# Optimization experiments

Measured on AMD Instinct MI355X. Metric: run time of the kernel, lower is better.

The kernel has to match this reference:

```python
import jax, jax.numpy as jnp
import numpy as np

NUM_QUERIES = 150
NEG = 1e9


def setup_inputs() -> dict:
    key = jax.random.key(0)
    ks = jax.random.split(key, 5)
    B, C, H, W = 4, 256, 64, 64
    img_feat = jax.random.normal(ks[0], (B, C, H, W), dtype=jnp.float32)
    exe_feat = jax.random.normal(ks[1], (B, C), dtype=jnp.float32)
    mask = jax.random.bernoulli(ks[2], 0.9, (B, H, W)).astype(jnp.float32)
    # similarity initialized as identity (plus tiny noise so it's non-degenerate)
    similarity = jnp.eye(C, dtype=jnp.float32) + 0.01 * jax.random.normal(ks[3], (C, C), dtype=jnp.float32)
    # nn.Linear weight, shape (out, in)
    v_w = jax.random.normal(ks[4], (C, C), dtype=jnp.float32) / np.sqrt(C)
    return {"img_feat": img_feat, "exe_feat": exe_feat, "mask": mask,
            "similarity": similarity, "v_w": v_w}


def _get_queries(attn, B, H, W):
    # peak detection on similarity-to-exemplar channel (last column), no grad
    simil = jax.lax.stop_gradient(attn[:, :, -1]).reshape(B, H, W)
    c = simil[:, 1:-1, 1:-1]
    is_max = ((c > simil[:, :-2, 1:-1]) &   # strictly greater than above
              (c >= simil[:, 2:, 1:-1]) &   # >= below
              (c > simil[:, 1:-1, :-2]) &   # strictly greater than left
              (c >= simil[:, 1:-1, 2:]))    # >= right
    pen = jnp.zeros_like(simil).at[:, 1:-1, 1:-1].set(
        jnp.where(is_max, 0.0, NEG))
    scores = (simil - pen).reshape(B, H * W)
    _, q_ids = jax.lax.top_k(scores, NUM_QUERIES)  # [B, Q]
    return q_ids


def reference(img_feat, exe_feat, mask, similarity, v_w):
    B, C, H, W = img_feat.shape
    HW = H * W
    unrolled = img_feat.reshape(B, C, HW)                      # [B,C,HW]
    exe = (exe_feat * 1.2)[:, :, None]                         # [B,C,1]
    concat = jnp.concatenate([unrolled, exe], axis=2)          # [B,C,HW+1]
    # values = Linear(concat^T): x @ W^T
    values = jnp.einsum('bcn,dc->bnd', concat, v_w)            # [B,HW+1,C]
    # attn = unrolled^T @ similarity @ concat
    attn = jnp.einsum('bcn,cd,bdm->bnm', unrolled, similarity, concat)  # [B,HW,HW+1]

    q_ids = _get_queries(attn, B, H, W)                        # [B,Q] int
    queries = jnp.take_along_axis(values[:, :-1], q_ids[:, :, None], axis=1)  # [B,Q,C]

    # masked softmax: outer product of pixel mask, exemplar column always kept
    m = jax.lax.stop_gradient(mask).reshape(B, HW)
    mm = m[:, :, None] * m[:, None, :]                         # [B,HW,HW]
    mm = jnp.concatenate([mm, jnp.ones((B, HW, 1), mm.dtype)], axis=2)
    attn = attn - (mm != 1).astype(attn.dtype) * NEG
    attn = jax.nn.softmax(attn, axis=2)

    new_img = jnp.einsum('bnm,bmd->bnd', attn, values)         # [B,HW,C]
    new_img = new_img.transpose(0, 2, 1).reshape(B, C, H, W)
    return new_img + img_feat, queries
```

## Files before the change

### kernel.cpp

```cpp
#include <hip/hip_runtime.h>

#define CC   256
#define HWS  4096
#define MPAD 4160
#define NB   4
#define NTIL 65

typedef __attribute__((ext_vector_type(8))) short   short8;
typedef __attribute__((ext_vector_type(4))) float   floatx4;

static __device__ __forceinline__ short8 ld8(const unsigned short* p) {
  return *(const short8*)p;
}
static __device__ __forceinline__ void st8(unsigned short* p, short8 v) {
  *(short8*)p = v;
}
static __device__ __forceinline__ unsigned short f2b(float x) {
  union { float f; unsigned u; } v; v.f = x;
  unsigned r = v.u + 0x7FFFu + ((v.u >> 16) & 1u);
  return (unsigned short)(r >> 16);
}
static __device__ __forceinline__ float b2f(unsigned short x) {
  union { unsigned u; float f; } v; v.u = ((unsigned)x) << 16;
  return v.f;
}

__global__ void prep_colb(const float* __restrict__ sim, const float* __restrict__ vw,
                          const float* __restrict__ mask,
                          unsigned short* __restrict__ St, unsigned short* __restrict__ Vw,
                          float* __restrict__ colb) {
  int blk = blockIdx.x, tid = threadIdx.x;
  if (blk < CC) {
    int dd = blk, c = tid;
    St[dd*CC + c] = f2b(sim[c*CC + dd]);
    Vw[dd*CC + c] = f2b(vw[dd*CC + c]);
    return;
  }
  int b = blk - CC;
  for (int m = tid; m < MPAD; m += 256) {
    float v;
    if (m < HWS)      v = (mask[b*HWS + m] - 1.0f) * 1e9f;
    else if (m == HWS) v = 0.0f;
    else               v = -3.0e38f;
    colb[b*MPAD + m] = v;
  }
}

__global__ void build_kt(const float* __restrict__ img, const float* __restrict__ exe,
                         unsigned short* __restrict__ Kt, unsigned short* __restrict__ Kf) {
  int b = blockIdx.x, mt = blockIdx.y, dt = blockIdx.z;
  int tid = threadIdx.x;
  int m0 = mt*64, d0 = dt*64;
  int w = tid >> 6, lane = tid & 63, lo = lane & 15, hi = lane >> 4;
  unsigned short* kft = Kf + (size_t)(b*NTIL + mt)*16384;
  if (mt == 64) {
    for (int i = 0; i < 16; ++i) {
      int m = m0 + (tid>>6) + i*4;
      int d = d0 + (tid&63);
      unsigned short v = 0;
      if (m == 4096) v = f2b(1.2f * exe[b*CC + d]);
      Kt[((size_t)b*MPAD + m)*CC + d] = v;
    }
#pragma unroll
    for (int ss = 0; ss < 2; ++ss) {
      int s = dt*8 + w*2 + ss;
      int k = s >> 2, t = s & 3;
      unsigned short tmp[8] = {0,0,0,0,0,0,0,0};
      if (t == 0 && lo == 0) {
#pragma unroll
        for (int j = 0; j < 8; ++j)
          tmp[j] = f2b(1.2f * exe[b*CC + k*32 + hi*8 + j]);
      }
      st8(kft + s*512 + lane*8, *(short8*)tmp);
    }
    return;
  }
  __shared__ float tile[64][65];
  for (int i = 0; i < 16; ++i) {
    int dl = (tid>>6) + i*4, ml = tid&63;
    tile[dl][ml] = img[((size_t)b*CC + d0+dl)*HWS + m0+ml];
  }
  __syncthreads();
  for (int i = 0; i < 16; ++i) {
    int ml = (tid>>6) + i*4, dl = tid&63;
    Kt[((size_t)b*MPAD + m0+ml)*CC + d0+dl] = f2b(tile[dl][ml]);
  }
#pragma unroll
  for (int ss = 0; ss < 2; ++ss) {
    int s = dt*8 + w*2 + ss;
    int k = s >> 2, t = s & 3;
    int ml = t*16 + lo;
    int dlb = (k - dt*2)*32 + hi*8;
    unsigned short tmp[8];
#pragma unroll
    for (int j = 0; j < 8; ++j) tmp[j] = f2b(tile[dlb + j][ml]);
    st8(kft + s*512 + lane*8, *(short8*)tmp);
  }
}

__global__ __launch_bounds__(256) void gemm_small(const unsigned short* __restrict__ Kt,
    const unsigned short* __restrict__ Bm, unsigned short* __restrict__ Tout,
    unsigned short* __restrict__ Vf, int mode) {
  int b  = blockIdx.x;
  int r0 = blockIdx.y*64 + (threadIdx.x>>6)*16;
  int c0 = blockIdx.z*64;
  int lane = threadIdx.x & 63;
  int lo = lane & 15, hi = lane >> 4;
  floatx4 acc[4] = {};
  const unsigned short* arow = Kt + ((size_t)b*MPAD + r0 + lo)*CC + hi*8;
#pragma unroll
  for (int k = 0; k < 8; ++k) {
    short8 af = ld8(arow + k*32);
#pragma unroll
    for (int t = 0; t < 4; ++t) {
      short8 bf = ld8(Bm + (size_t)(c0 + t*16 + lo)*CC + k*32 + hi*8);
      acc[t] = __builtin_amdgcn_mfma_f32_16x16x32_bf16(af, bf, acc[t], 0, 0, 0);
    }
  }
  if (mode == 0) {
#pragma unroll
    for (int t = 0; t < 4; ++t)
#pragma unroll
      for (int r = 0; r < 4; ++r) {
        int n = r0 + hi*4 + r, dd = c0 + t*16 + lo;
        Tout[((size_t)b*HWS + n)*CC + dd] = f2b(acc[t][r]);
      }
  } else {
    unsigned short* vfb = Vf + (size_t)b*NTIL*16384;
#pragma unroll
    for (int t = 0; t < 4; ++t)
#pragma unroll
      for (int r = 0; r < 4; ++r) {
        int m = r0 + hi*4 + r, dd = c0 + t*16 + lo;
        int mt = m >> 6, ml = m & 63;
        int h = ml >> 5, im = ml & 31;
        int s = h*16 + (dd >> 4);
        int lane2 = (im >> 3)*16 + lo;
        int j = im & 7;
        vfb[(size_t)mt*16384 + s*512 + lane2*8 + j] = f2b(acc[t][r]);
      }
  }
}

__global__ __launch_bounds__(256) void scores_kernel(const float* __restrict__ img,
    const float* __restrict__ sim, const float* __restrict__ exe,
    float* __restrict__ score32) {
  int b = blockIdx.x, n0 = blockIdx.y*32;
  int d = threadIdx.x;
  __shared__ float U[32][257];
  __shared__ float R[32][257];
  __shared__ float E[256];
  for (int idx = threadIdx.x; idx < 32*256; idx += 256) {
    int nl = idx & 31, c = idx >> 5;
    U[nl][c] = img[((size_t)b*CC + c)*HWS + n0 + nl];
  }
  E[d] = 1.2f * exe[b*CC + d];
  __syncthreads();
  float acc[32];
#pragma unroll
  for (int nl = 0; nl < 32; ++nl) acc[nl] = 0.f;
  for (int c = 0; c < CC; ++c) {
    float s_cd = sim[c*CC + d];
#pragma unroll
    for (int nl = 0; nl < 32; ++nl) acc[nl] = fmaf(U[nl][c], s_cd, acc[nl]);
  }
#pragma unroll
  for (int nl = 0; nl < 32; ++nl) R[nl][d] = acc[nl];
  __syncthreads();
  if (d < 32) {
    float s = 0.f;
    for (int dd = 0; dd < CC; ++dd) s = fmaf(R[d][dd], E[dd], s);
    score32[b*HWS + n0 + d] = s;
  }
}

__global__ __launch_bounds__(64) void select_kernel(const float* __restrict__ scores,
                                                    int* __restrict__ qids) {
  int b = blockIdx.x, lane = threadIdx.x;
  __shared__ float sc[HWS];
  __shared__ unsigned long long kx[HWS];
  __shared__ unsigned long long list[256];
  __shared__ unsigned int hist[256];
  __shared__ unsigned int st[4];
  __shared__ unsigned long long sh_base;

  const floatx4* s4 = (const floatx4*)(scores + (size_t)b*HWS);
  floatx4* c4 = (floatx4*)sc;
#pragma unroll
  for (int i = 0; i < 16; ++i) c4[i*64 + lane] = s4[i*64 + lane];
  __syncthreads();

  for (int i = 0; i < 64; ++i) {
    int idx = i*64 + lane;
    int y = i, x = lane;
    float c0 = sc[idx];
    float v = c0;
    if (y >= 1 && y <= 62 && x >= 1 && x <= 62) {
      bool ismax = (c0 > sc[idx-64]) && (c0 >= sc[idx+64]) &&
                   (c0 > sc[idx-1])  && (c0 >= sc[idx+1]);
      if (!ismax) v = c0 - 1e9f;
    }
    unsigned u = __float_as_uint(v);
    u = (u & 0x80000000u) ? ~u : (u | 0x80000000u);
    kx[idx] = (((unsigned long long)u) << 12) | (unsigned long long)(4095 - idx);
  }
  __syncthreads();

  unsigned long long base = 0;
  unsigned int need = 150, C = 0;
  for (int s = 36; s >= 4; s -= 8) {
    for (int i = lane; i < 256; i += 64) hist[i] = 0;
    __syncthreads();
    unsigned long long pref = base >> (s + 8);
    for (int i = 0; i < 64; ++i) {
      unsigned long long k = kx[i*64 + lane];
      if ((k >> (s + 8)) == pref) atomicAdd(&hist[(unsigned)(k >> s) & 255u], 1u);
    }
    __syncthreads();
    if (lane == 0) {
      unsigned cum = 0; int B = 0;
      for (int bin = 255; bin >= 0; --bin) {
        cum += hist[bin];
        if (cum >= need) { B = bin; break; }
      }
      st[0] = (150u - need) + cum;
      st[1] = need - (cum - hist[B]);
      sh_base = base | ((unsigned long long)B << s);
    }
    __syncthreads();
    C = st[0]; need = st[1]; base = sh_base;
    if (C <= 256u) break;
  }

  if (lane == 0) st[2] = 0;
  __syncthreads();
  for (int i = 0; i < 64; ++i) {
    unsigned long long k = kx[i*64 + lane];
    if (k >= base) {
      unsigned p = atomicAdd(&st[2], 1u);
      list[p] = k;
    }
  }
  __syncthreads();
  for (int i = lane; i < 256; i += 64) if (i >= (int)C) list[i] = 0ull;
  __syncthreads();

  for (int kk = 2; kk <= 256; kk <<= 1) {
    for (int j = kk >> 1; j > 0; j >>= 1) {
#pragma unroll
      for (int tt = 0; tt < 2; ++tt) {
        int t = lane + tt*64;
        int i2 = ((t & ~(j - 1)) << 1) | (t & (j - 1));
        int p2 = i2 | j;
        bool desc = ((i2 & kk) == 0);
        unsigned long long a = list[i2], c = list[p2];
        bool sw = desc ? (a < c) : (a > c);
        if (sw) { list[i2] = c; list[p2] = a; }
      }
      __syncthreads();
    }
  }

  for (int q = lane; q < 150; q += 64)
    qids[b*150 + q] = 4095 - (int)(list[q] & 0xFFFull);
}

__global__ __launch_bounds__(256, 1) void flash_kernel(
    const unsigned short* __restrict__ Tb, const unsigned short* __restrict__ Kt,
    const unsigned short* __restrict__ Kf, const unsigned short* __restrict__ Vf,
    const float* __restrict__ mask, const float* __restrict__ colb,
    float* __restrict__ acc0, float* __restrict__ accH, float* __restrict__ lsums) {
  int blk = blockIdx.x;
  int b    = (blk & 7) >> 1;
  int half = blk & 1;
  int g    = blk >> 3;
  int tid = threadIdx.x;
  int wave = tid >> 6, lane = tid & 63;
  int lo = lane & 15, hi = lane >> 4;
  int n0 = g*128 + wave*32;
  int t0 = half ? 33 : 0, t1 = half ? NTIL : 33;

  __shared__ unsigned short pbuf[4][1152];
  unsigned short* plw = &pbuf[wave][0];

  short8 q0[8], q1[8];
  const unsigned short* tb0 = Tb + ((size_t)b*HWS + n0 + lo)*CC + hi*8;
#pragma unroll
  for (int k = 0; k < 8; ++k) { q0[k] = ld8(tb0 + k*32); q1[k] = ld8(tb0 + 16*CC + k*32); }

  const unsigned short* kfb = Kf + (size_t)b*NTIL*16384 + lane*8;
  const unsigned short* vfb = Vf + (size_t)b*NTIL*16384 + lane*8;

  short8 X[16], Y[16];
#pragma unroll
  for (int i = 0; i < 16; ++i) X[i] = ld8(kfb + (size_t)t0*16384 + i*512);
#pragma unroll
  for (int i = 0; i < 16; ++i) Y[i] = ld8(kfb + (size_t)t0*16384 + (16 + i)*512);

  const float* mk = mask + b*HWS;

  float crb0[4], Msub0[4], crb1[4], Msub1[4];
  {
    const unsigned short* kep = Kt + ((size_t)b*MPAD + HWS)*CC + hi*8;
    float ddot = 0.f, edot = 0.f;
    const unsigned short* kdp = Kt + ((size_t)b*MPAD + n0 + lo)*CC + hi*8;
#pragma unroll
    for (int k = 0; k < 8; ++k) {
      short8 kd = ld8(kdp + k*32);
      short8 ke = ld8(kep + k*32);
#pragma unroll
      for (int j = 0; j < 8; ++j) {
        float qf = b2f((unsigned short)q0[k][j]);
        ddot = fmaf(qf, b2f((unsigned short)kd[j]), ddot);
        edot = fmaf(qf, b2f((unsigned short)ke[j]), edot);
      }
    }
    ddot += __shfl_xor(ddot, 16); ddot += __shfl_xor(ddot, 32);
    edot += __shfl_xor(edot, 16); edot += __shfl_xor(edot, 32);
    float Mrow = ((mk[n0 + lo] == 1.0f) ? ddot : edot) + 2.0f;
    float* fM = (float*)plw;
    fM[lo] = Mrow;
#pragma unroll
    for (int r = 0; r < 4; ++r) {
      Msub0[r] = fM[hi*4 + r];
      crb0[r]  = (mk[n0 + hi*4 + r] - 1.0f)*1e9f - Msub0[r];
    }
    ddot = 0.f; edot = 0.f;
    const unsigned short* kdp1 = Kt + ((size_t)b*MPAD + n0 + 16 + lo)*CC + hi*8;
#pragma unroll
    for (int k = 0; k < 8; ++k) {
      short8 kd = ld8(kdp1 + k*32);
      short8 ke = ld8(kep + k*32);
#pragma unroll
      for (int j = 0; j < 8; ++j) {
        float qf = b2f((unsigned short)q1[k][j]);
        ddot = fmaf(qf, b2f((unsigned short)kd[j]), ddot);
        edot = fmaf(qf, b2f((unsigned short)ke[j]), edot);
      }
    }
    ddot += __shfl_xor(ddot, 16); ddot += __shfl_xor(ddot, 32);
    edot += __shfl_xor(edot, 16); edot += __shfl_xor(edot, 32);
    float Mrow1 = ((mk[n0 + 16 + lo] == 1.0f) ? ddot : edot) + 2.0f;
    fM[lo] = Mrow1;
#pragma unroll
    for (int r = 0; r < 4; ++r) {
      Msub1[r] = fM[hi*4 + r];
      crb1[r]  = (mk[n0 + 16 + hi*4 + r] - 1.0f)*1e9f - Msub1[r];
    }
  }

  float lsum0[4] = {0.f, 0.f, 0.f, 0.f};
  float lsum1[4] = {0.f, 0.f, 0.f, 0.f};
  floatx4 o0[16] = {};
  floatx4 o1[16] = {};
  const float* cbb = colb + b*MPAD;

  for (int mt = t0; mt < t1; ++mt) {
    int m0 = mt*64;
    const unsigned short* vs = vfb + (size_t)mt*16384;
    floatx4 s0[4] = {}, s1[4] = {};
#pragma unroll
    for (int k = 0; k < 4; ++k)
#pragma unroll
      for (int t = 0; t < 4; ++t) {
        s0[t] = __builtin_amdgcn_mfma_f32_16x16x32_bf16(q0[k], X[k*4 + t], s0[t], 0, 0, 0);
        s1[t] = __builtin_amdgcn_mfma_f32_16x16x32_bf16(q1[k], X[k*4 + t], s1[t], 0, 0, 0);
      }
#pragma unroll
    for (int i = 0; i < 16; ++i) X[i] = ld8(vs + i*512);
#pragma unroll
    for (int k = 4; k < 8; ++k)
#pragma unroll
      for (int t = 0; t < 4; ++t) {
        s0[t] = __builtin_amdgcn_mfma_f32_16x16x32_bf16(q0[k], Y[(k-4)*4 + t], s0[t], 0, 0, 0);
        s1[t] = __builtin_amdgcn_mfma_f32_16x16x32_bf16(q1[k], Y[(k-4)*4 + t], s1[t], 0, 0, 0);
      }
#pragma unroll
    for (int i = 0; i < 16; ++i) Y[i] = ld8(vs + (16 + i)*512);
    float cb[4];
#pragma unroll
    for (int t = 0; t < 4; ++t) cb[t] = cbb[m0 + t*16 + lo];
    short8 pf00, pf01, pf10, pf11;
    {
      float pr[4][4];
#pragma unroll
      for (int t = 0; t < 4; ++t)
#pragma unroll
        for (int r = 0; r < 4; ++r)
          pr[t][r] = s0[t][r] + cb[t] + crb0[r];
      if (mt == NTIL-1 && lo == 0) {
#pragma unroll
        for (int r = 0; r < 4; ++r) pr[0][r] = s0[0][r] - Msub0[r];
      }
#pragma unroll
      for (int t = 0; t < 4; ++t)
#pragma unroll
        for (int r = 0; r < 4; ++r) {
          float p = __expf(pr[t][r]);
          lsum0[r] += p;
          plw[(hi*4 + r)*72 + t*16 + lo] = f2b(p);
        }
      pf00 = *(const short8*)&plw[lo*72 + hi*8];
      pf01 = *(const short8*)&plw[lo*72 + 32 + hi*8];
    }
    {
      float pr[4][4];
#pragma unroll
      for (int t = 0; t < 4; ++t)
#pragma unroll
        for (int r = 0; r < 4; ++r)
          pr[t][r] = s1[t][r] + cb[t] + crb1[r];
      if (mt == NTIL-1 && lo == 0) {
#pragma unroll
        for (int r = 0; r < 4; ++r) pr[0][r] = s1[0][r] - Msub1[r];
      }
#pragma unroll
      for (int t = 0; t < 4; ++t)
#pragma unroll
        for (int r = 0; r < 4; ++r) {
          float p = __expf(pr[t][r]);
          lsum1[r] += p;
          plw[(hi*4 + r)*72 + t*16 + lo] = f2b(p);
        }
      pf10 = *(const short8*)&plw[lo*72 + hi*8];
      pf11 = *(const short8*)&plw[lo*72 + 32 + hi*8];
    }
#pragma unroll
    for (int sl = 0; sl < 16; ++sl) {
      o0[sl] = __builtin_amdgcn_mfma_f32_16x16x32_bf16(pf00, X[sl], o0[sl], 0, 0, 0);
      o1[sl] = __builtin_amdgcn_mfma_f32_16x16x32_bf16(pf10, X[sl], o1[sl], 0, 0, 0);
    }
    if (mt + 1 < t1) {
      const unsigned short* ks = kfb + (size_t)(mt+1)*16384;
#pragma unroll
      for (int i = 0; i < 16; ++i) X[i] = ld8(ks + i*512);
    }
#pragma unroll
    for (int sl = 0; sl < 16; ++sl) {
      o0[sl] = __builtin_amdgcn_mfma_f32_16x16x32_bf16(pf01, Y[sl], o0[sl], 0, 0, 0);
      o1[sl] = __builtin_amdgcn_mfma_f32_16x16x32_bf16(pf11, Y[sl], o1[sl], 0, 0, 0);
    }
    if (mt + 1 < t1) {
      const unsigned short* ks = kfb + (size_t)(mt+1)*16384;
#pragma unroll
      for (int i = 0; i < 16; ++i) Y[i] = ld8(ks + (16 + i)*512);
    }
  }
#pragma unroll
  for (int r = 0; r < 4; ++r) {
#pragma unroll
    for (int off = 1; off < 16; off <<= 1) {
      lsum0[r] += __shfl_xor(lsum0[r], off);
      lsum1[r] += __shfl_xor(lsum1[r], off);
    }
  }
  float* op = (half ? accH : acc0) + (size_t)b*CC*HWS;
#pragma unroll
  for (int t = 0; t < 16; ++t)
#pragma unroll
    for (int r = 0; r < 4; ++r) {
      op[(size_t)(t*16 + lo)*HWS + n0 + hi*4 + r]      = o0[t][r];
      op[(size_t)(t*16 + lo)*HWS + n0 + 16 + hi*4 + r] = o1[t][r];
    }
  if (lo == 0) {
    float* lp = lsums + ((size_t)(half*NB + b))*HWS;
#pragma unroll
    for (int r = 0; r < 4; ++r) {
      lp[n0 + hi*4 + r]      = lsum0[r];
      lp[n0 + 16 + hi*4 + r] = lsum1[r];
    }
  }
}

__global__ __launch_bounds__(256) void finalize_kernel(const float* __restrict__ accH,
    const float* __restrict__ lsums, const float* __restrict__ img,
    float* __restrict__ out0) {
  int b = blockIdx.x >> 8;
  int d = blockIdx.x & 255;
  size_t base = ((size_t)b*CC + d)*HWS;
  const float* l0 = lsums + (size_t)b*HWS;
  const float* l1 = lsums + (size_t)(NB + b)*HWS;
  for (int n = threadIdx.x; n < HWS; n += 256) {
    float inv = 1.0f / (l0[n] + l1[n]);
    float o = (out0[base + n] + accH[base + n]) * inv;
    out0[base + n] = b2f(f2b(o)) + img[base + n];
  }
}

__global__ __launch_bounds__(256) void gather_kernel(const float* __restrict__ img,
    const float* __restrict__ vw, const int* __restrict__ qids, float* __restrict__ out1) {
  int blk = blockIdx.x;
  int b = blk / 150, q = blk % 150;
  int dd = threadIdx.x;
  __shared__ float col[CC];
  int id = qids[b*150 + q];
  col[dd] = img[((size_t)b*CC + dd)*HWS + id];
  __syncthreads();
  const float* vr = vw + dd*CC;
  float acc = 0.f;
  for (int c = 0; c < CC; ++c) acc = fmaf(col[c], vr[c], acc);
  out1[((size_t)(b*150 + q))*CC + dd] = acc;
}

extern "C" void kernel_launch(void* const* d_in, const int* in_sizes, int n_in,
                              void* d_out, int out_size, void* d_ws, size_t ws_size,
                              hipStream_t stream) {
  const float* img  = (const float*)d_in[0];
  const float* exe  = (const float*)d_in[1];
  const float* mask = (const float*)d_in[2];
  const float* sim  = (const float*)d_in[3];
  const float* vw   = (const float*)d_in[4];
  float* out0 = (float*)d_out;
  float* out1 = out0 + (size_t)NB*CC*HWS;

  char* ws = (char*)d_ws;
  size_t o = 0;
  unsigned short* Kt  = (unsigned short*)(ws + o); o += (size_t)NB*MPAD*CC*2;
  unsigned short* Tb  = (unsigned short*)(ws + o); o += (size_t)NB*HWS*CC*2;
  unsigned short* Kf  = (unsigned short*)(ws + o); o += (size_t)NB*NTIL*16384*2;
  unsigned short* Vf  = (unsigned short*)(ws + o); o += (size_t)NB*NTIL*16384*2;
  unsigned short* St  = (unsigned short*)(ws + o); o += (size_t)CC*CC*2;
  unsigned short* Vw  = (unsigned short*)(ws + o); o += (size_t)CC*CC*2;
  float*          scores = (float*)(ws + o);       o += (size_t)NB*HWS*4;
  float*          colb   = (float*)(ws + o);       o += (size_t)NB*MPAD*4;
  int*            qids   = (int*)(ws + o);         o += (size_t)NB*150*4;
  float*          accH   = (float*)(ws + o);       o += (size_t)NB*CC*HWS*4;
  float*          lsums  = (float*)(ws + o);       o += (size_t)2*NB*HWS*4;

  prep_colb  <<<dim3(CC + NB),    dim3(256), 0, stream>>>(sim, vw, mask, St, Vw, colb);
  build_kt   <<<dim3(NB, 65, 4),  dim3(256), 0, stream>>>(img, exe, Kt, Kf);
  gemm_small <<<dim3(NB, 64, 4),  dim3(256), 0, stream>>>(Kt, St, Tb, nullptr, 0);
  gemm_small <<<dim3(NB, 65, 4),  dim3(256), 0, stream>>>(Kt, Vw, nullptr, Vf, 1);
  scores_kernel<<<dim3(NB, 128),  dim3(256), 0, stream>>>(img, sim, exe, scores);
  select_kernel<<<dim3(NB),       dim3(64),  0, stream>>>(scores, qids);
  flash_kernel <<<dim3(256),      dim3(256), 0, stream>>>(Tb, Kt, Kf, Vf, mask, colb,
                                                          out0, accH, lsums);
  finalize_kernel<<<dim3(NB*CC),  dim3(256), 0, stream>>>(accH, lsums, img, out0);
  gather_kernel<<<dim3(NB*150),   dim3(256), 0, stream>>>(img, vw, qids, out1);
}
```

Before: 375.4 us.

## Stage gemm_small outputs through LDS and restructure K/V register prefetch pipeline

gemm_small now writes its MFMA accumulators into a shared-memory tile and then emits coalesced 16-byte stores, for both the row-major T output and the fragment-packed V layout. Before, each thread did scattered 2-byte global stores. In the attention loop, the whole K tile (32 fragments) is held in registers and prefetched one tile ahead. V is loaded in two halves, the second half fetched just before it is used. This reorders how memory latency overlaps with the QK and PV MFMAs, at the cost of higher register pressure (48 short8 operand registers instead of 32), which may lower occupancy or cause spills.

```diff
diff --git a/kernel.cpp b/kernel.cpp
--- a/kernel.cpp
+++ b/kernel.cpp
@@ -102,10 +102,13 @@
     const unsigned short* __restrict__ Bm, unsigned short* __restrict__ Tout,
     unsigned short* __restrict__ Vf, int mode) {
   int b  = blockIdx.x;
-  int r0 = blockIdx.y*64 + (threadIdx.x>>6)*16;
+  int by = blockIdx.y;
+  int w  = threadIdx.x >> 6;
+  int r0 = by*64 + w*16;
   int c0 = blockIdx.z*64;
   int lane = threadIdx.x & 63;
   int lo = lane & 15, hi = lane >> 4;
+  __shared__ unsigned short lsh[64][72];
   floatx4 acc[4] = {};
   const unsigned short* arow = Kt + ((size_t)b*MPAD + r0 + lo)*CC + hi*8;
 #pragma unroll
@@ -121,24 +124,30 @@
 #pragma unroll
     for (int t = 0; t < 4; ++t)
 #pragma unroll
-      for (int r = 0; r < 4; ++r) {
-        int n = r0 + hi*4 + r, dd = c0 + t*16 + lo;
-        Tout[((size_t)b*HWS + n)*CC + dd] = f2b(acc[t][r]);
-      }
+      for (int r = 0; r < 4; ++r)
+        lsh[w*16 + hi*4 + r][t*16 + lo] = f2b(acc[t][r]);
+    __syncthreads();
+    int tid = threadIdx.x;
+    int nl = tid >> 2, seg = tid & 3;
+    unsigned short* dst = Tout + ((size_t)b*HWS + by*64 + nl)*CC + c0 + seg*16;
+    st8(dst,     ld8(&lsh[nl][seg*16]));
+    st8(dst + 8, ld8(&lsh[nl][seg*16 + 8]));
   } else {
-    unsigned short* vfb = Vf + (size_t)b*NTIL*16384;
 #pragma unroll
     for (int t = 0; t < 4; ++t)
 #pragma unroll
-      for (int r = 0; r < 4; ++r) {
-        int m = r0 + hi*4 + r, dd = c0 + t*16 + lo;
-        int mt = m >> 6, ml = m & 63;
-        int h = ml >> 5, im = ml & 31;
-        int s = h*16 + (dd >> 4);
-        int lane2 = (im >> 3)*16 + lo;
-        int j = im & 7;
-        vfb[(size_t)mt*16384 + s*512 + lane2*8 + j] = f2b(acc[t][r]);
-      }
+      for (int r = 0; r < 4; ++r)
+        lsh[t*16 + lo][w*16 + hi*4 + r] = f2b(acc[t][r]);
+    __syncthreads();
+    unsigned short* vfb2 = Vf + (size_t)(b*NTIL + by)*16384;
+#pragma unroll
+    for (int ss = 0; ss < 2; ++ss) {
+      int idx = w*2 + ss;
+      int h = idx >> 2, t4 = idx & 3;
+      int s = h*16 + (c0 >> 4) + t4;
+      short8 v = ld8(&lsh[t4*16 + (lane & 15)][h*32 + (lane >> 4)*8]);
+      st8(vfb2 + s*512 + lane*8, v);
+    }
   }
 }
 
@@ -291,11 +300,11 @@
   const unsigned short* kfb = Kf + (size_t)b*NTIL*16384 + lane*8;
   const unsigned short* vfb = Vf + (size_t)b*NTIL*16384 + lane*8;
 
-  short8 X[16], Y[16];
-#pragma unroll
-  for (int i = 0; i < 16; ++i) X[i] = ld8(kfb + (size_t)t0*16384 + i*512);
-#pragma unroll
-  for (int i = 0; i < 16; ++i) Y[i] = ld8(kfb + (size_t)t0*16384 + (16 + i)*512);
+  short8 ka[32], X[16];
+#pragma unroll
+  for (int i = 0; i < 32; ++i) ka[i] = ld8(kfb + (size_t)t0*16384 + i*512);
+#pragma unroll
+  for (int i = 0; i < 16; ++i) X[i] = ld8(vfb + (size_t)t0*16384 + i*512);
 
   const float* mk = mask + b*HWS;
 
@@ -357,26 +366,19 @@
 
   for (int mt = t0; mt < t1; ++mt) {
     int m0 = mt*64;
-    const unsigned short* vs = vfb + (size_t)mt*16384;
     floatx4 s0[4] = {}, s1[4] = {};
 #pragma unroll
-    for (int k = 0; k < 4; ++k)
+    for (int k = 0; k < 8; ++k)
 #pragma unroll
       for (int t = 0; t < 4; ++t) {
-        s0[t] = __builtin_amdgcn_mfma_f32_16x16x32_bf16(q0[k], X[k*4 + t], s0[t], 0, 0, 0);
-        s1[t] = __builtin_amdgcn_mfma_f32_16x16x32_bf16(q1[k], X[k*4 + t], s1[t], 0, 0, 0);
-      }
-#pragma unroll
-    for (int i = 0; i < 16; ++i) X[i] = ld8(vs + i*512);
-#pragma unroll
-    for (int k = 4; k < 8; ++k)
-#pragma unroll
-      for (int t = 0; t < 4; ++t) {
-        s0[t] = __builtin_amdgcn_mfma_f32_16x16x32_bf16(q0[k], Y[(k-4)*4 + t], s0[t], 0, 0, 0);
-        s1[t] = __builtin_amdgcn_mfma_f32_16x16x32_bf16(q1[k], Y[(k-4)*4 + t], s1[t], 0, 0, 0);
-      }
-#pragma unroll
-    for (int i = 0; i < 16; ++i) Y[i] = ld8(vs + (16 + i)*512);
+        s0[t] = __builtin_amdgcn_mfma_f32_16x16x32_bf16(q0[k], ka[k*4 + t], s0[t], 0, 0, 0);
+        s1[t] = __builtin_amdgcn_mfma_f32_16x16x32_bf16(q1[k], ka[k*4 + t], s1[t], 0, 0, 0);
+      }
+    if (mt + 1 < t1) {
+      const unsigned short* ks = kfb + (size_t)(mt+1)*16384;
+#pragma unroll
+      for (int i = 0; i < 32; ++i) ka[i] = ld8(ks + i*512);
+    }
     float cb[4];
 #pragma unroll
     for (int t = 0; t < 4; ++t) cb[t] = cbb[m0 + t*16 + lo];
@@ -430,20 +432,20 @@
       o0[sl] = __builtin_amdgcn_mfma_f32_16x16x32_bf16(pf00, X[sl], o0[sl], 0, 0, 0);
       o1[sl] = __builtin_amdgcn_mfma_f32_16x16x32_bf16(pf10, X[sl], o1[sl], 0, 0, 0);
     }
+    {
+      const unsigned short* vs = vfb + (size_t)mt*16384;
+#pragma unroll
+      for (int i = 0; i < 16; ++i) X[i] = ld8(vs + (16 + i)*512);
+    }
+#pragma unroll
+    for (int sl = 0; sl < 16; ++sl) {
+      o0[sl] = __builtin_amdgcn_mfma_f32_16x16x32_bf16(pf01, X[sl], o0[sl], 0, 0, 0);
+      o1[sl] = __builtin_amdgcn_mfma_f32_16x16x32_bf16(pf11, X[sl], o1[sl], 0, 0, 0);
+    }
     if (mt + 1 < t1) {
-      const unsigned short* ks = kfb + (size_t)(mt+1)*16384;
-#pragma unroll
-      for (int i = 0; i < 16; ++i) X[i] = ld8(ks + i*512);
-    }
-#pragma unroll
-    for (int sl = 0; sl < 16; ++sl) {
-      o0[sl] = __builtin_amdgcn_mfma_f32_16x16x32_bf16(pf01, Y[sl], o0[sl], 0, 0, 0);
-      o1[sl] = __builtin_amdgcn_mfma_f32_16x16x32_bf16(pf11, Y[sl], o1[sl], 0, 0, 0);
-    }
-    if (mt + 1 < t1) {
-      const unsigned short* ks = kfb + (size_t)(mt+1)*16384;
-#pragma unroll
-      for (int i = 0; i < 16; ++i) Y[i] = ld8(ks + (16 + i)*512);
+      const unsigned short* vsn = vfb + (size_t)(mt+1)*16384;
+#pragma unroll
+      for (int i = 0; i < 16; ++i) X[i] = ld8(vsn + i*512);
     }
   }
 #pragma unroll
```

After: 608.6 us. 1.62x slower.
